# Kernel optimization log

Hardware: AMD Instinct MI355X
Metric: run time of the kernel (lower is better)

## Reference

```python
import jax, jax.numpy as jnp
import numpy as np

B, N_L, N_T, C_IN, HID, NG, ATOMS, N_EDGES = 8, 128, 512, 128, 128, 10, 24, 4096
BN_EPS = 1e-5


def setup_inputs() -> dict:
    key = jax.random.key(0)
    ks = jax.random.split(key, 20)
    f32 = jnp.float32
    s = 0.05  # weight scale
    return {
        "h_l_x": jax.random.normal(ks[0], (B, N_L, C_IN), f32),
        "h_t_x": jax.random.normal(ks[1], (B, N_T, C_IN), f32),
        "l_mask": jnp.ones((B, N_L), dtype=bool),
        "t_mask": jnp.ones((B, N_T), dtype=bool),
        "h_l_pos": jax.random.normal(ks[2], (B, N_L, 3), f32),
        "h_t_pos": jax.random.normal(ks[3], (B, N_T * ATOMS, 3), f32),
        "x_l_flat": jax.random.normal(ks[4], (B * N_L, C_IN), f32),
        "edge_index": jax.random.randint(ks[5], (2, N_EDGES), 0, B * N_L),
        "W1": jax.random.normal(ks[6], (2 * C_IN, HID), f32) * s,
        "b1": jnp.zeros((HID,), f32),
        "bn_gamma": jnp.ones((HID,), f32),
        "bn_beta": jnp.zeros((HID,), f32),
        "bn_mean": jnp.zeros((HID,), f32),
        "bn_var": jnp.ones((HID,), f32),
        "W_pi": jax.random.normal(ks[7], (HID, NG), f32) * s,
        "b_pi": jnp.zeros((NG,), f32),
        "W_sigma": jax.random.normal(ks[8], (HID, NG), f32) * s,
        "b_sigma": jnp.zeros((NG,), f32),
        "W_mu": jax.random.normal(ks[9], (HID, NG), f32) * s,
        "b_mu": jnp.zeros((NG,), f32),
        "W_nuc": jax.random.normal(ks[10], (C_IN, 12), f32) * s,
        "b_nuc": jnp.zeros((12,), f32),
        "W_bond": jax.random.normal(ks[11], (2 * C_IN, 4), f32) * s,
        "b_bond": jnp.zeros((4,), f32),
    }


def reference(h_l_x, h_t_x, l_mask, t_mask, h_l_pos, h_t_pos, x_l_flat, edge_index,
              W1, b1, bn_gamma, bn_beta, bn_mean, bn_var,
              W_pi, b_pi, W_sigma, b_sigma, W_mu, b_mu,
              W_nuc, b_nuc, W_bond, b_bond):
    Bsz, Nl, Cd = h_l_x.shape
    Nt = h_t_x.shape[1]
    # dense pairwise concat: [B, N_l, N_t, 2C] (masks are all-True, so the
    # boolean selection C[C_mask] of the original is a static flatten)
    pair = jnp.concatenate([
        jnp.broadcast_to(h_l_x[:, :, None, :], (Bsz, Nl, Nt, Cd)),
        jnp.broadcast_to(h_t_x[:, None, :, :], (Bsz, Nl, Nt, Cd)),
    ], axis=-1).reshape(-1, 2 * Cd)
    # MLP: Linear -> BatchNorm1d (eval, running stats) -> ELU -> Dropout(eval=id)
    h = pair @ W1 + b1
    h = (h - bn_mean) * jax.lax.rsqrt(bn_var + BN_EPS) * bn_gamma + bn_beta
    h = jax.nn.elu(h)
    # MDN heads
    pi = jax.nn.softmax(h @ W_pi + b_pi, axis=-1)
    sigma = jax.nn.elu(h @ W_sigma + b_sigma) + 1.1
    mu = jax.nn.elu(h @ W_mu + b_mu) + 1.0
    # auxiliary heads on flat ligand node features
    nuc_types = x_l_flat @ W_nuc + b_nuc
    bond_feat = jnp.concatenate([x_l_flat[edge_index[0]], x_l_flat[edge_index[1]]], axis=1)
    bond_types = bond_feat @ W_bond + b_bond
    # pairwise distances with windowed min over 24 atoms per target residue
    d2 = (-2.0 * jnp.einsum('bld,btd->blt', h_l_pos, h_t_pos)
          + jnp.sum(h_t_pos ** 2, axis=-1)[:, None, :]
          + jnp.sum(h_l_pos ** 2, axis=-1)[:, :, None])
    d = jnp.nan_to_num(jnp.sqrt(d2), nan=10000.0)  # nan from sqrt(<0)
    dist = d.reshape(Bsz, Nl, Nt, ATOMS).min(axis=-1)  # [B, N_l, N_t]
    dist = jax.lax.stop_gradient(dist.reshape(-1)[:, None])  # detached, [M,1]
    C_batch = jnp.broadcast_to(jnp.arange(Bsz)[:, None, None], (Bsz, Nl, Nt)).reshape(-1)
    return (pi, sigma, mu, dist, nuc_types, bond_types, C_batch)
```

## Files before the change

### kernel.cpp

```cpp
#include <hip/hip_runtime.h>

#define B_      8
#define N_L     128
#define N_T     512
#define C_IN    128
#define HID     128
#define NG      10
#define ATOMS   24
#define N_EDGES 4096

#define OFF_PI  0
#define OFF_SG  5242880
#define OFF_MU  10485760
#define OFF_DI  15728640
#define OFF_NU  16252928
#define OFF_BO  16265216
#define OFF_CB  16281600

#define WS_U    0
#define WS_V    131072
#define WS_W    655360
#define WS_B    659456
#define WS_WT   659488

typedef unsigned short u16;
typedef unsigned int   u32;
typedef short s16x8 __attribute__((ext_vector_type(8)));
typedef float f32x4 __attribute__((ext_vector_type(4)));
typedef u32   u32x4 __attribute__((ext_vector_type(4)));

__device__ __forceinline__ float bfu2f(u16 s) {
  u32 u = ((u32)s) << 16;
  return __builtin_bit_cast(float, u);
}
__device__ __forceinline__ u16 f2bf(float f) {
  u32 u = __builtin_bit_cast(u32, f);
  u32 r = (u + 0x7fffu + ((u >> 16) & 1u)) >> 16;
  return (u16)r;
}
__device__ __forceinline__ u32 pack2(float a, float b) {
  return (u32)f2bf(a) | ((u32)f2bf(b) << 16);
}
__device__ __forceinline__ u32 pkhi(float hi, float lo) {
  return __builtin_amdgcn_perm(__builtin_bit_cast(u32, hi),
                               __builtin_bit_cast(u32, lo), 0x07060302u);
}
__device__ __forceinline__ float eluf(float x) {
  return x > 0.f ? x : __expf(x) - 1.f;
}
__device__ __forceinline__ s16x8 ld8(const u16* p) {
  return __builtin_bit_cast(s16x8, *(const u32x4*)p);
}

template<bool F32>
__device__ __forceinline__ float ldf(const void* p, size_t i) {
  if constexpr (F32) return ((const float*)p)[i];
  else               return bfu2f(((const u16*)p)[i]);
}
template<bool F32>
__device__ __forceinline__ u16 wraw(const void* p, size_t i) {
  if constexpr (F32) return f2bf(((const float*)p)[i]);
  else               return ((const u16*)p)[i];
}
__device__ __forceinline__ bool is_f32(const u32* probe) {
  return (probe[0] & 0xFFFFu) == 0u;
}

template<bool F32>
__device__ __forceinline__ void prep_impl(
    const void* hlx, const void* htx, const void* W1, const void* b1,
    const void* gam, const void* bet, const void* mean_, const void* var_,
    const void* Wpi, const void* bpi, const void* Wsg, const void* bsg,
    const void* Wmu, const void* bmu, float* __restrict__ ws,
    float* __restrict__ xr) {
  int blk = blockIdx.x;
  int k = threadIdx.x;
  float A = ldf<F32>(gam, k) * rsqrtf(ldf<F32>(var_, k) + 1e-5f);
  if (blk < 5120) {
    const void* x; size_t xoff, woff; float* dst; bool isU = (blk < 1024);
    if (isU) { x = hlx; xoff = (size_t)blk * C_IN; woff = 0;
               dst = ws + WS_U + blk * HID; }
    else     { int r = blk - 1024; x = htx; xoff = (size_t)r * C_IN;
               woff = (size_t)C_IN * HID; dst = ws + WS_V + r * HID; }
    xr[k] = ldf<F32>(x, xoff + k);
    __syncthreads();
    float acc = 0.f;
    #pragma unroll 4
    for (int c = 0; c < C_IN; ++c) acc += xr[c] * ldf<F32>(W1, woff + (size_t)c * HID + k);
    float r = acc * A;
    if (isU) r += ldf<F32>(b1, k) * A + (ldf<F32>(bet, k) - ldf<F32>(mean_, k) * A);
    dst[k] = r;
  } else {
    for (int j = 0; j < 32; ++j) {
      float wv = 0.f;
      if (j < 10)      wv = ldf<F32>(Wpi, (size_t)k * NG + j);
      else if (j < 20) wv = ldf<F32>(Wsg, (size_t)k * NG + j - 10);
      else if (j < 30) wv = ldf<F32>(Wmu, (size_t)k * NG + j - 20);
      ws[WS_W + k * 32 + j] = wv;
    }
    u16* wt = (u16*)(ws + WS_WT);
    for (int j = 0; j < 32; ++j) {
      u16 val = 0;
      if (j < 10)      val = wraw<F32>(Wpi, (size_t)k * NG + j);
      else if (j < 20) val = wraw<F32>(Wsg, (size_t)k * NG + j - 10);
      else if (j < 30) val = wraw<F32>(Wmu, (size_t)k * NG + j - 20);
      wt[(size_t)j * HID + k] = val;
    }
    if (k < 32) {
      float bb = 0.f;
      if (k < 10)      bb = ldf<F32>(bpi, k);
      else if (k < 20) bb = ldf<F32>(bsg, k - 10);
      else if (k < 30) bb = ldf<F32>(bmu, k - 20);
      ws[WS_B + k] = bb;
    }
  }
}

__global__ __launch_bounds__(128) void prep_kernel(
    const void* hlx, const void* htx, const void* W1, const void* b1,
    const void* gam, const void* bet, const void* mean_, const void* var_,
    const void* Wpi, const void* bpi, const void* Wsg, const void* bsg,
    const void* Wmu, const void* bmu, float* ws, const u32* probe) {
  __shared__ float xr[C_IN];
  if (is_f32(probe))
    prep_impl<true >(hlx, htx, W1, b1, gam, bet, mean_, var_, Wpi, bpi, Wsg, bsg, Wmu, bmu, ws, xr);
  else
    prep_impl<false>(hlx, htx, W1, b1, gam, bet, mean_, var_, Wpi, bpi, Wsg, bsg, Wmu, bmu, ws, xr);
}

__global__ __launch_bounds__(256) void main_pairs(const float* __restrict__ ws,
                                                  void* __restrict__ out,
                                                  const u32* probe) {
  int tid = threadIdx.x;
  int lane = tid & 63, wave = tid >> 6;
  int p = lane & 15, q = lane >> 4;
  int bl = blockIdx.x >> 2, tq = blockIdx.x & 3;
  int b = bl >> 7;
  bool f32o = is_f32(probe);

  const u16* wt = (const u16*)(ws + WS_WT);
  s16x8 wf0[4], wf1[4];
  #pragma unroll
  for (int kt = 0; kt < 4; ++kt) {
    wf0[kt] = ld8(wt + (size_t)p        * HID + kt*32 + q*8);
    wf1[kt] = ld8(wt + (size_t)(16 + p) * HID + kt*32 + q*8);
  }
  const float* up = ws + WS_U + (size_t)bl * HID;
  float ue[4][8];
  #pragma unroll
  for (int kt = 0; kt < 4; ++kt) {
    f32x4 a0 = *(const f32x4*)(up + kt*32 + q*8);
    f32x4 a1 = *(const f32x4*)(up + kt*32 + q*8 + 4);
    #pragma unroll
    for (int i = 0; i < 4; ++i) { ue[kt][i] = a0[i]; ue[kt][4+i] = a1[i]; }
  }
  float bias0[4], bias1[4];
  #pragma unroll
  for (int r = 0; r < 4; ++r) {
    bias0[r] = ws[WS_B + q*4 + r];
    bias1[r] = ws[WS_B + 16 + q*4 + r];
  }

  for (int tt = 0; tt < 2; ++tt) {
    int t = tq * 128 + wave * 32 + tt * 16 + p;
    const float* vp = ws + WS_V + (size_t)(b * N_T + t) * HID;
    f32x4 acc0 = {0.f,0.f,0.f,0.f}, acc1 = {0.f,0.f,0.f,0.f};
    #pragma unroll
    for (int kt = 0; kt < 4; ++kt) {
      f32x4 va = *(const f32x4*)(vp + kt*32 + q*8);
      f32x4 vb = *(const f32x4*)(vp + kt*32 + q*8 + 4);
      float h0 = eluf(va[0] + ue[kt][0]);
      float h1 = eluf(va[1] + ue[kt][1]);
      float h2 = eluf(va[2] + ue[kt][2]);
      float h3 = eluf(va[3] + ue[kt][3]);
      float h4 = eluf(vb[0] + ue[kt][4]);
      float h5 = eluf(vb[1] + ue[kt][5]);
      float h6 = eluf(vb[2] + ue[kt][6]);
      float h7 = eluf(vb[3] + ue[kt][7]);
      u32x4 hw = { pkhi(h1,h0), pkhi(h3,h2), pkhi(h5,h4), pkhi(h7,h6) };
      s16x8 hf = __builtin_bit_cast(s16x8, hw);
      acc0 = __builtin_amdgcn_mfma_f32_16x16x32_bf16(wf0[kt], hf, acc0, 0, 0, 0);
      acc1 = __builtin_amdgcn_mfma_f32_16x16x32_bf16(wf1[kt], hf, acc1, 0, 0, 0);
    }
    float v0[4], v1[4];
    #pragma unroll
    for (int r = 0; r < 4; ++r) { v0[r] = acc0[r] + bias0[r]; v1[r] = acc1[r] + bias1[r]; }
    float pm = -3.0e38f;
    #pragma unroll
    for (int r = 0; r < 4; ++r) if (q*4 + r < 10) pm = fmaxf(pm, v0[r]);
    pm = fmaxf(pm, __shfl_xor(pm, 16));
    pm = fmaxf(pm, __shfl_xor(pm, 32));
    float e[4]; float es = 0.f;
    #pragma unroll
    for (int r = 0; r < 4; ++r) {
      e[r] = 0.f;
      if (q*4 + r < 10) { e[r] = __expf(v0[r] - pm); es += e[r]; }
    }
    es += __shfl_xor(es, 16);
    es += __shfl_xor(es, 32);
    float inv = 1.f / es;
    size_t base = ((size_t)bl * N_T + t) * NG;

    if (f32o) {
      float* o = (float*)out;
      if (q == 0) {
        *(float2*)(o + OFF_PI + base + 0) = make_float2(e[0]*inv, e[1]*inv);
        *(float2*)(o + OFF_PI + base + 2) = make_float2(e[2]*inv, e[3]*inv);
        *(float2*)(o + OFF_SG + base + 6) = make_float2(eluf(v1[0])+1.1f, eluf(v1[1])+1.1f);
        *(float2*)(o + OFF_SG + base + 8) = make_float2(eluf(v1[2])+1.1f, eluf(v1[3])+1.1f);
      } else if (q == 1) {
        *(float2*)(o + OFF_PI + base + 4) = make_float2(e[0]*inv, e[1]*inv);
        *(float2*)(o + OFF_PI + base + 6) = make_float2(e[2]*inv, e[3]*inv);
        *(float2*)(o + OFF_MU + base + 0) = make_float2(eluf(v1[0])+1.0f, eluf(v1[1])+1.0f);
        *(float2*)(o + OFF_MU + base + 2) = make_float2(eluf(v1[2])+1.0f, eluf(v1[3])+1.0f);
      } else if (q == 2) {
        *(float2*)(o + OFF_PI + base + 8) = make_float2(e[0]*inv, e[1]*inv);
        *(float2*)(o + OFF_SG + base + 0) = make_float2(eluf(v0[2])+1.1f, eluf(v0[3])+1.1f);
        *(float2*)(o + OFF_MU + base + 4) = make_float2(eluf(v1[0])+1.0f, eluf(v1[1])+1.0f);
        *(float2*)(o + OFF_MU + base + 6) = make_float2(eluf(v1[2])+1.0f, eluf(v1[3])+1.0f);
      } else {
        *(float2*)(o + OFF_SG + base + 2) = make_float2(eluf(v0[0])+1.1f, eluf(v0[1])+1.1f);
        *(float2*)(o + OFF_SG + base + 4) = make_float2(eluf(v0[2])+1.1f, eluf(v0[3])+1.1f);
        *(float2*)(o + OFF_MU + base + 8) = make_float2(eluf(v1[0])+1.0f, eluf(v1[1])+1.0f);
      }
    } else {
      u16* o = (u16*)out;
      if (q == 0) {
        *(u32*)(o + OFF_PI + base + 0) = pack2(e[0]*inv, e[1]*inv);
        *(u32*)(o + OFF_PI + base + 2) = pack2(e[2]*inv, e[3]*inv);
        *(u32*)(o + OFF_SG + base + 6) = pack2(eluf(v1[0])+1.1f, eluf(v1[1])+1.1f);
        *(u32*)(o + OFF_SG + base + 8) = pack2(eluf(v1[2])+1.1f, eluf(v1[3])+1.1f);
      } else if (q == 1) {
        *(u32*)(o + OFF_PI + base + 4) = pack2(e[0]*inv, e[1]*inv);
        *(u32*)(o + OFF_PI + base + 6) = pack2(e[2]*inv, e[3]*inv);
        *(u32*)(o + OFF_MU + base + 0) = pack2(eluf(v1[0])+1.0f, eluf(v1[1])+1.0f);
        *(u32*)(o + OFF_MU + base + 2) = pack2(eluf(v1[2])+1.0f, eluf(v1[3])+1.0f);
      } else if (q == 2) {
        *(u32*)(o + OFF_PI + base + 8) = pack2(e[0]*inv, e[1]*inv);
        *(u32*)(o + OFF_SG + base + 0) = pack2(eluf(v0[2])+1.1f, eluf(v0[3])+1.1f);
        *(u32*)(o + OFF_MU + base + 4) = pack2(eluf(v1[0])+1.0f, eluf(v1[1])+1.0f);
        *(u32*)(o + OFF_MU + base + 6) = pack2(eluf(v1[2])+1.0f, eluf(v1[3])+1.0f);
      } else {
        *(u32*)(o + OFF_SG + base + 2) = pack2(eluf(v0[0])+1.1f, eluf(v0[1])+1.1f);
        *(u32*)(o + OFF_SG + base + 4) = pack2(eluf(v0[2])+1.1f, eluf(v0[3])+1.1f);
        *(u32*)(o + OFF_MU + base + 8) = pack2(eluf(v1[0])+1.0f, eluf(v1[1])+1.0f);
      }
    }
  }
}

template<bool F32>
__device__ __forceinline__ void dist_impl(const void* __restrict__ lpos,
                                          const void* __restrict__ tpos,
                                          void* __restrict__ out) {
  int blk = blockIdx.x;
  int lc   = blk & 31;
  int half = (blk >> 5) & 1;
  int b    = blk >> 6;
  int t = half * 256 + threadIdx.x;

  size_t tbase = ((size_t)b * (N_T * ATOMS) + (size_t)t * ATOMS) * 3;
  float ax[ATOMS], ay[ATOMS], az[ATOMS], an[ATOMS];
  if constexpr (F32) {
    float c[72];
    const float4* tp4 = (const float4*)((const float*)tpos + tbase);
    #pragma unroll
    for (int i = 0; i < 18; ++i) {
      float4 qv = tp4[i];
      c[4*i+0] = qv.x; c[4*i+1] = qv.y; c[4*i+2] = qv.z; c[4*i+3] = qv.w;
    }
    #pragma unroll
    for (int a = 0; a < ATOMS; ++a) {
      ax[a] = c[3*a]; ay[a] = c[3*a+1]; az[a] = c[3*a+2];
      an[a] = ax[a]*ax[a] + ay[a]*ay[a] + az[a]*az[a];
    }
  } else {
    u32 raw[36];
    const uint4* tp4 = (const uint4*)((const u16*)tpos + tbase);
    #pragma unroll
    for (int i = 0; i < 9; ++i) {
      uint4 qv = tp4[i];
      raw[4*i+0] = qv.x; raw[4*i+1] = qv.y; raw[4*i+2] = qv.z; raw[4*i+3] = qv.w;
    }
    #pragma unroll
    for (int a = 0; a < ATOMS; ++a) {
      int e = 3 * a;
      u32 w0 = raw[e >> 1];
      ax[a] = bfu2f((e & 1) ? (u16)(w0 >> 16) : (u16)w0);
      u32 w1 = raw[(e + 1) >> 1];
      ay[a] = bfu2f(((e + 1) & 1) ? (u16)(w1 >> 16) : (u16)w1);
      u32 w2 = raw[(e + 2) >> 1];
      az[a] = bfu2f(((e + 2) & 1) ? (u16)(w2 >> 16) : (u16)w2);
      an[a] = ax[a]*ax[a] + ay[a]*ay[a] + az[a]*az[a];
    }
  }
  #pragma unroll
  for (int il = 0; il < 4; ++il) {
    int l = lc * 4 + il;
    size_t lbase = ((size_t)b * N_L + l) * 3;
    float lx = ldf<F32>(lpos, lbase), ly = ldf<F32>(lpos, lbase+1), lz = ldf<F32>(lpos, lbase+2);
    float ln = lx*lx + ly*ly + lz*lz;
    float m = 1e30f;
    #pragma unroll
    for (int a = 0; a < ATOMS; ++a) {
      float dot = ax[a]*lx + ay[a]*ly + az[a]*lz;
      float d2 = ln + an[a] - 2.f * dot;
      d2 = (d2 >= 0.f) ? d2 : 1e30f;
      m = fminf(m, d2);
    }
    float d = (m < 1e29f) ? sqrtf(m) : 10000.0f;
    long p = ((long)(b * N_L + l)) * N_T + t;
    if constexpr (F32) {
      ((float*)out)[OFF_DI + p] = d;
      ((float*)out)[OFF_CB + p] = (float)b;
    } else {
      ((u16*)out)[OFF_DI + p] = f2bf(d);
      ((u16*)out)[OFF_CB + p] = f2bf((float)b);
    }
  }
}

__global__ __launch_bounds__(256) void dist_kernel(const void* lpos, const void* tpos,
                                                   void* out, const u32* probe) {
  if (is_f32(probe)) dist_impl<true >(lpos, tpos, out);
  else               dist_impl<false>(lpos, tpos, out);
}

template<bool F32>
__device__ __forceinline__ void aux_impl(const void* __restrict__ xl,
                                         const int* __restrict__ eidx,
                                         const void* __restrict__ Wnu, const void* __restrict__ bnu,
                                         const void* __restrict__ Wbo, const void* __restrict__ bbo,
                                         void* __restrict__ out) {
  int gid = blockIdx.x * 256 + threadIdx.x;
  if (gid < 1024 * 12) {
    int r = gid / 12, j = gid - r * 12;
    float acc = ldf<F32>(bnu, j);
    for (int c = 0; c < C_IN; ++c)
      acc += ldf<F32>(xl, (size_t)r * C_IN + c) * ldf<F32>(Wnu, (size_t)c * 12 + j);
    if constexpr (F32) ((float*)out)[OFF_NU + gid] = acc;
    else               ((u16*)out)[OFF_NU + gid] = f2bf(acc);
  } else if (gid < 1024 * 12 + N_EDGES * 4) {
    int g = gid - 1024 * 12;
    int e = g >> 2, j = g & 3;
    int e0 = eidx[e], e1 = eidx[N_EDGES + e];
    float acc = ldf<F32>(bbo, j);
    for (int c = 0; c < C_IN; ++c)
      acc += ldf<F32>(xl, (size_t)e0 * C_IN + c) * ldf<F32>(Wbo, (size_t)c * 4 + j);
    for (int c = 0; c < C_IN; ++c)
      acc += ldf<F32>(xl, (size_t)e1 * C_IN + c) * ldf<F32>(Wbo, (size_t)(C_IN + c) * 4 + j);
    if constexpr (F32) ((float*)out)[OFF_BO + g] = acc;
    else               ((u16*)out)[OFF_BO + g] = f2bf(acc);
  }
}

__global__ __launch_bounds__(256) void aux_kernel(const void* xl, const int* eidx,
                                                  const void* Wnu, const void* bnu,
                                                  const void* Wbo, const void* bbo,
                                                  void* out, const u32* probe) {
  if (is_f32(probe)) aux_impl<true >(xl, eidx, Wnu, bnu, Wbo, bbo, out);
  else               aux_impl<false>(xl, eidx, Wnu, bnu, Wbo, bbo, out);
}

extern "C" void kernel_launch(void* const* d_in, const int* in_sizes, int n_in,
                              void* d_out, int out_size, void* d_ws, size_t ws_size,
                              hipStream_t stream) {
  int s = (n_in >= 24) ? 2 : 0;
  const void* hlx  = d_in[0];
  const void* htx  = d_in[1];
  const void* lpos = d_in[2 + s];
  const void* tpos = d_in[3 + s];
  const void* xl   = d_in[4 + s];
  const int*  eidx = (const int*)d_in[5 + s];
  const void* W1   = d_in[6 + s];
  const void* b1   = d_in[7 + s];
  const void* gam  = d_in[8 + s];
  const void* bet  = d_in[9 + s];
  const void* mean_= d_in[10 + s];
  const void* var_ = d_in[11 + s];
  const void* Wpi  = d_in[12 + s];
  const void* bpi  = d_in[13 + s];
  const void* Wsg  = d_in[14 + s];
  const void* bsg  = d_in[15 + s];
  const void* Wmu  = d_in[16 + s];
  const void* bmu  = d_in[17 + s];
  const void* Wnu  = d_in[18 + s];
  const void* bnu  = d_in[19 + s];
  const void* Wbo  = d_in[20 + s];
  const void* bbo  = d_in[21 + s];
  const u32* probe = (const u32*)var_;
  float* ws = (float*)d_ws;

  prep_kernel<<<5121, 128, 0, stream>>>(hlx, htx, W1, b1, gam, bet, mean_, var_,
                                        Wpi, bpi, Wsg, bsg, Wmu, bmu, ws, probe);
  main_pairs<<<4096, 256, 0, stream>>>(ws, d_out, probe);
  dist_kernel<<<512, 256, 0, stream>>>(lpos, tpos, d_out, probe);
  aux_kernel<<<(1024 * 12 + N_EDGES * 4 + 255) / 256, 256, 0, stream>>>(
      xl, eidx, Wnu, bnu, Wbo, bbo, d_out, probe);
}
```

Before: 204.5 us.

## Fuse four launches into two and restructure prep and aux heads

Merges the distance kernel into the prep launch and the nucleotide/bond heads into the main pair kernel, cutting four launches to two so the independent pieces can run together. The prep row projection now handles 8 rows per 256-thread block, so each W1 load is reused across four rows. The aux heads switch from one thread per output doing serial 128/256-length dots to one wave per row or edge using coalesced loads and shuffle reductions. The unused fp32 head-weight copy is dropped. In exchange, the fused launches mix block types with different register needs, which can lower occupancy for the main pair blocks.

```diff
diff --git a/kernel.cpp b/kernel.cpp
--- a/kernel.cpp
+++ b/kernel.cpp
@@ -19,7 +19,6 @@
 
 #define WS_U    0
 #define WS_V    131072
-#define WS_W    655360
 #define WS_B    659456
 #define WS_WT   659488
 
@@ -67,76 +66,233 @@
 }
 
 template<bool F32>
-__device__ __forceinline__ void prep_impl(
+__device__ __forceinline__ void prep_rows(
+    int blk, int tid,
+    const void* hlx, const void* htx, const void* W1, const void* b1,
+    const void* gam, const void* bet, const void* mean_, const void* var_,
+    float* __restrict__ ws, float (*xs)[C_IN]) {
+  int k = tid & 127, g = tid >> 7;
+  bool isU = (blk < 128);
+  const void* x = isU ? hlx : htx;
+  int row0 = isU ? blk * 8 : (blk - 128) * 8;
+  size_t woff = isU ? 0 : (size_t)C_IN * HID;
+  #pragma unroll
+  for (int i = 0; i < 4; ++i) {
+    int e = tid + i * 256;
+    int rr = e >> 7, cc = e & 127;
+    xs[rr][cc] = ldf<F32>(x, (size_t)(row0 + rr) * C_IN + cc);
+  }
+  __syncthreads();
+  float a0 = 0.f, a1 = 0.f, a2 = 0.f, a3 = 0.f;
+  const float* xr0 = xs[g * 4 + 0];
+  const float* xr1 = xs[g * 4 + 1];
+  const float* xr2 = xs[g * 4 + 2];
+  const float* xr3 = xs[g * 4 + 3];
+  #pragma unroll 8
+  for (int c = 0; c < C_IN; ++c) {
+    float w = ldf<F32>(W1, woff + (size_t)c * HID + k);
+    a0 += xr0[c] * w;
+    a1 += xr1[c] * w;
+    a2 += xr2[c] * w;
+    a3 += xr3[c] * w;
+  }
+  float A = ldf<F32>(gam, k) * rsqrtf(ldf<F32>(var_, k) + 1e-5f);
+  float add = 0.f;
+  if (isU) add = ldf<F32>(b1, k) * A + (ldf<F32>(bet, k) - ldf<F32>(mean_, k) * A);
+  float* dst = ws + (isU ? WS_U : WS_V) + (size_t)row0 * HID;
+  dst[(g * 4 + 0) * HID + k] = a0 * A + add;
+  dst[(g * 4 + 1) * HID + k] = a1 * A + add;
+  dst[(g * 4 + 2) * HID + k] = a2 * A + add;
+  dst[(g * 4 + 3) * HID + k] = a3 * A + add;
+}
+
+template<bool F32>
+__device__ __forceinline__ void prep_consts(
+    int tid, const void* Wpi, const void* bpi, const void* Wsg, const void* bsg,
+    const void* Wmu, const void* bmu, float* __restrict__ ws) {
+  if (tid >= 128) return;
+  int k = tid;
+  u16* wt = (u16*)(ws + WS_WT);
+  for (int j = 0; j < 32; ++j) {
+    u16 val = 0;
+    if (j < 10)      val = wraw<F32>(Wpi, (size_t)k * NG + j);
+    else if (j < 20) val = wraw<F32>(Wsg, (size_t)k * NG + j - 10);
+    else if (j < 30) val = wraw<F32>(Wmu, (size_t)k * NG + j - 20);
+    wt[(size_t)j * HID + k] = val;
+  }
+  if (k < 32) {
+    float bb = 0.f;
+    if (k < 10)      bb = ldf<F32>(bpi, k);
+    else if (k < 20) bb = ldf<F32>(bsg, k - 10);
+    else if (k < 30) bb = ldf<F32>(bmu, k - 20);
+    ws[WS_B + k] = bb;
+  }
+}
+
+template<bool F32>
+__device__ __forceinline__ void dist_impl(int blk2,
+                                          const void* __restrict__ lpos,
+                                          const void* __restrict__ tpos,
+                                          void* __restrict__ out) {
+  int lc   = blk2 & 31;
+  int half = (blk2 >> 5) & 1;
+  int b    = blk2 >> 6;
+  int t = half * 256 + threadIdx.x;
+
+  size_t tbase = ((size_t)b * (N_T * ATOMS) + (size_t)t * ATOMS) * 3;
+  float ax[ATOMS], ay[ATOMS], az[ATOMS], an[ATOMS];
+  if constexpr (F32) {
+    float c[72];
+    const float4* tp4 = (const float4*)((const float*)tpos + tbase);
+    #pragma unroll
+    for (int i = 0; i < 18; ++i) {
+      float4 qv = tp4[i];
+      c[4*i+0] = qv.x; c[4*i+1] = qv.y; c[4*i+2] = qv.z; c[4*i+3] = qv.w;
+    }
+    #pragma unroll
+    for (int a = 0; a < ATOMS; ++a) {
+      ax[a] = c[3*a]; ay[a] = c[3*a+1]; az[a] = c[3*a+2];
+      an[a] = ax[a]*ax[a] + ay[a]*ay[a] + az[a]*az[a];
+    }
+  } else {
+    u32 raw[36];
+    const uint4* tp4 = (const uint4*)((const u16*)tpos + tbase);
+    #pragma unroll
+    for (int i = 0; i < 9; ++i) {
+      uint4 qv = tp4[i];
+      raw[4*i+0] = qv.x; raw[4*i+1] = qv.y; raw[4*i+2] = qv.z; raw[4*i+3] = qv.w;
+    }
+    #pragma unroll
+    for (int a = 0; a < ATOMS; ++a) {
+      int e = 3 * a;
+      u32 w0 = raw[e >> 1];
+      ax[a] = bfu2f((e & 1) ? (u16)(w0 >> 16) : (u16)w0);
+      u32 w1 = raw[(e + 1) >> 1];
+      ay[a] = bfu2f(((e + 1) & 1) ? (u16)(w1 >> 16) : (u16)w1);
+      u32 w2 = raw[(e + 2) >> 1];
+      az[a] = bfu2f(((e + 2) & 1) ? (u16)(w2 >> 16) : (u16)w2);
+      an[a] = ax[a]*ax[a] + ay[a]*ay[a] + az[a]*az[a];
+    }
+  }
+  #pragma unroll
+  for (int il = 0; il < 4; ++il) {
+    int l = lc * 4 + il;
+    size_t lbase = ((size_t)b * N_L + l) * 3;
+    float lx = ldf<F32>(lpos, lbase), ly = ldf<F32>(lpos, lbase+1), lz = ldf<F32>(lpos, lbase+2);
+    float ln = lx*lx + ly*ly + lz*lz;
+    float m = 1e30f;
+    #pragma unroll
+    for (int a = 0; a < ATOMS; ++a) {
+      float dot = ax[a]*lx + ay[a]*ly + az[a]*lz;
+      float d2 = ln + an[a] - 2.f * dot;
+      d2 = (d2 >= 0.f) ? d2 : 1e30f;
+      m = fminf(m, d2);
+    }
+    float d = (m < 1e29f) ? sqrtf(m) : 10000.0f;
+    long p = ((long)(b * N_L + l)) * N_T + t;
+    if constexpr (F32) {
+      ((float*)out)[OFF_DI + p] = d;
+      ((float*)out)[OFF_CB + p] = (float)b;
+    } else {
+      ((u16*)out)[OFF_DI + p] = f2bf(d);
+      ((u16*)out)[OFF_CB + p] = f2bf((float)b);
+    }
+  }
+}
+
+__global__ __launch_bounds__(256) void prep_fused(
     const void* hlx, const void* htx, const void* W1, const void* b1,
     const void* gam, const void* bet, const void* mean_, const void* var_,
     const void* Wpi, const void* bpi, const void* Wsg, const void* bsg,
-    const void* Wmu, const void* bmu, float* __restrict__ ws,
-    float* __restrict__ xr) {
+    const void* Wmu, const void* bmu, float* ws,
+    const void* lpos, const void* tpos, void* out, const u32* probe) {
+  __shared__ float xs[8][C_IN];
   int blk = blockIdx.x;
-  int k = threadIdx.x;
-  float A = ldf<F32>(gam, k) * rsqrtf(ldf<F32>(var_, k) + 1e-5f);
-  if (blk < 5120) {
-    const void* x; size_t xoff, woff; float* dst; bool isU = (blk < 1024);
-    if (isU) { x = hlx; xoff = (size_t)blk * C_IN; woff = 0;
-               dst = ws + WS_U + blk * HID; }
-    else     { int r = blk - 1024; x = htx; xoff = (size_t)r * C_IN;
-               woff = (size_t)C_IN * HID; dst = ws + WS_V + r * HID; }
-    xr[k] = ldf<F32>(x, xoff + k);
-    __syncthreads();
-    float acc = 0.f;
-    #pragma unroll 4
-    for (int c = 0; c < C_IN; ++c) acc += xr[c] * ldf<F32>(W1, woff + (size_t)c * HID + k);
-    float r = acc * A;
-    if (isU) r += ldf<F32>(b1, k) * A + (ldf<F32>(bet, k) - ldf<F32>(mean_, k) * A);
-    dst[k] = r;
+  int tid = threadIdx.x;
+  bool f = is_f32(probe);
+  if (blk < 640) {
+    if (f) prep_rows<true >(blk, tid, hlx, htx, W1, b1, gam, bet, mean_, var_, ws, xs);
+    else   prep_rows<false>(blk, tid, hlx, htx, W1, b1, gam, bet, mean_, var_, ws, xs);
+  } else if (blk == 640) {
+    if (f) prep_consts<true >(tid, Wpi, bpi, Wsg, bsg, Wmu, bmu, ws);
+    else   prep_consts<false>(tid, Wpi, bpi, Wsg, bsg, Wmu, bmu, ws);
   } else {
-    for (int j = 0; j < 32; ++j) {
-      float wv = 0.f;
-      if (j < 10)      wv = ldf<F32>(Wpi, (size_t)k * NG + j);
-      else if (j < 20) wv = ldf<F32>(Wsg, (size_t)k * NG + j - 10);
-      else if (j < 30) wv = ldf<F32>(Wmu, (size_t)k * NG + j - 20);
-      ws[WS_W + k * 32 + j] = wv;
-    }
-    u16* wt = (u16*)(ws + WS_WT);
-    for (int j = 0; j < 32; ++j) {
-      u16 val = 0;
-      if (j < 10)      val = wraw<F32>(Wpi, (size_t)k * NG + j);
-      else if (j < 20) val = wraw<F32>(Wsg, (size_t)k * NG + j - 10);
-      else if (j < 30) val = wraw<F32>(Wmu, (size_t)k * NG + j - 20);
-      wt[(size_t)j * HID + k] = val;
-    }
-    if (k < 32) {
-      float bb = 0.f;
-      if (k < 10)      bb = ldf<F32>(bpi, k);
-      else if (k < 20) bb = ldf<F32>(bsg, k - 10);
-      else if (k < 30) bb = ldf<F32>(bmu, k - 20);
-      ws[WS_B + k] = bb;
-    }
-  }
-}
-
-__global__ __launch_bounds__(128) void prep_kernel(
-    const void* hlx, const void* htx, const void* W1, const void* b1,
-    const void* gam, const void* bet, const void* mean_, const void* var_,
-    const void* Wpi, const void* bpi, const void* Wsg, const void* bsg,
-    const void* Wmu, const void* bmu, float* ws, const u32* probe) {
-  __shared__ float xr[C_IN];
-  if (is_f32(probe))
-    prep_impl<true >(hlx, htx, W1, b1, gam, bet, mean_, var_, Wpi, bpi, Wsg, bsg, Wmu, bmu, ws, xr);
-  else
-    prep_impl<false>(hlx, htx, W1, b1, gam, bet, mean_, var_, Wpi, bpi, Wsg, bsg, Wmu, bmu, ws, xr);
-}
-
-__global__ __launch_bounds__(256) void main_pairs(const float* __restrict__ ws,
-                                                  void* __restrict__ out,
-                                                  const u32* probe) {
+    int blk2 = blk - 641;
+    if (f) dist_impl<true >(blk2, lpos, tpos, out);
+    else   dist_impl<false>(blk2, lpos, tpos, out);
+  }
+}
+
+template<bool F32>
+__device__ __forceinline__ void nuc_wave(int r, int lane, const void* __restrict__ xl,
+    const void* __restrict__ Wnu, const void* __restrict__ bnu, void* __restrict__ out) {
+  float x0 = ldf<F32>(xl, (size_t)r * C_IN + lane);
+  float x1 = ldf<F32>(xl, (size_t)r * C_IN + 64 + lane);
+  #pragma unroll
+  for (int j = 0; j < 12; ++j) {
+    float a = x0 * ldf<F32>(Wnu, (size_t)lane * 12 + j)
+            + x1 * ldf<F32>(Wnu, (size_t)(64 + lane) * 12 + j);
+    #pragma unroll
+    for (int m = 32; m >= 1; m >>= 1) a += __shfl_xor(a, m);
+    if (lane == 0) {
+      float v = a + ldf<F32>(bnu, j);
+      if constexpr (F32) ((float*)out)[OFF_NU + (size_t)r * 12 + j] = v;
+      else               ((u16*)out)[OFF_NU + (size_t)r * 12 + j] = f2bf(v);
+    }
+  }
+}
+
+template<bool F32>
+__device__ __forceinline__ void bond_wave(int e, int lane, const void* __restrict__ xl,
+    const int* __restrict__ eidx, const void* __restrict__ Wbo,
+    const void* __restrict__ bbo, void* __restrict__ out) {
+  int e0 = eidx[e], e1 = eidx[N_EDGES + e];
+  float x0 = ldf<F32>(xl, (size_t)e0 * C_IN + lane);
+  float x1 = ldf<F32>(xl, (size_t)e0 * C_IN + 64 + lane);
+  float y0 = ldf<F32>(xl, (size_t)e1 * C_IN + lane);
+  float y1 = ldf<F32>(xl, (size_t)e1 * C_IN + 64 + lane);
+  #pragma unroll
+  for (int j = 0; j < 4; ++j) {
+    float a = x0 * ldf<F32>(Wbo, (size_t)lane * 4 + j)
+            + x1 * ldf<F32>(Wbo, (size_t)(64 + lane) * 4 + j)
+            + y0 * ldf<F32>(Wbo, (size_t)(128 + lane) * 4 + j)
+            + y1 * ldf<F32>(Wbo, (size_t)(192 + lane) * 4 + j);
+    #pragma unroll
+    for (int m = 32; m >= 1; m >>= 1) a += __shfl_xor(a, m);
+    if (lane == 0) {
+      float v = a + ldf<F32>(bbo, j);
+      if constexpr (F32) ((float*)out)[OFF_BO + (size_t)e * 4 + j] = v;
+      else               ((u16*)out)[OFF_BO + (size_t)e * 4 + j] = f2bf(v);
+    }
+  }
+}
+
+__global__ __launch_bounds__(256) void main_fused(
+    const float* __restrict__ ws, void* __restrict__ out, const u32* probe,
+    const void* __restrict__ xl, const int* __restrict__ eidx,
+    const void* __restrict__ Wnu, const void* __restrict__ bnu,
+    const void* __restrict__ Wbo, const void* __restrict__ bbo) {
+  int blk = blockIdx.x;
   int tid = threadIdx.x;
   int lane = tid & 63, wave = tid >> 6;
+  bool f32o = is_f32(probe);
+
+  if (blk >= 4096) {
+    if (blk < 4096 + 256) {
+      int r = (blk - 4096) * 4 + wave;
+      if (f32o) nuc_wave<true >(r, lane, xl, Wnu, bnu, out);
+      else      nuc_wave<false>(r, lane, xl, Wnu, bnu, out);
+    } else {
+      int e = (blk - 4352) * 4 + wave;
+      if (f32o) bond_wave<true >(e, lane, xl, eidx, Wbo, bbo, out);
+      else      bond_wave<false>(e, lane, xl, eidx, Wbo, bbo, out);
+    }
+    return;
+  }
+
   int p = lane & 15, q = lane >> 4;
-  int bl = blockIdx.x >> 2, tq = blockIdx.x & 3;
+  int bl = blk >> 2, tq = blk & 3;
   int b = bl >> 7;
-  bool f32o = is_f32(probe);
 
   const u16* wt = (const u16*)(ws + WS_WT);
   s16x8 wf0[4], wf1[4];
@@ -249,119 +405,6 @@
   }
 }
 
-template<bool F32>
-__device__ __forceinline__ void dist_impl(const void* __restrict__ lpos,
-                                          const void* __restrict__ tpos,
-                                          void* __restrict__ out) {
-  int blk = blockIdx.x;
-  int lc   = blk & 31;
-  int half = (blk >> 5) & 1;
-  int b    = blk >> 6;
-  int t = half * 256 + threadIdx.x;
-
-  size_t tbase = ((size_t)b * (N_T * ATOMS) + (size_t)t * ATOMS) * 3;
-  float ax[ATOMS], ay[ATOMS], az[ATOMS], an[ATOMS];
-  if constexpr (F32) {
-    float c[72];
-    const float4* tp4 = (const float4*)((const float*)tpos + tbase);
-    #pragma unroll
-    for (int i = 0; i < 18; ++i) {
-      float4 qv = tp4[i];
-      c[4*i+0] = qv.x; c[4*i+1] = qv.y; c[4*i+2] = qv.z; c[4*i+3] = qv.w;
-    }
-    #pragma unroll
-    for (int a = 0; a < ATOMS; ++a) {
-      ax[a] = c[3*a]; ay[a] = c[3*a+1]; az[a] = c[3*a+2];
-      an[a] = ax[a]*ax[a] + ay[a]*ay[a] + az[a]*az[a];
-    }
-  } else {
-    u32 raw[36];
-    const uint4* tp4 = (const uint4*)((const u16*)tpos + tbase);
-    #pragma unroll
-    for (int i = 0; i < 9; ++i) {
-      uint4 qv = tp4[i];
-      raw[4*i+0] = qv.x; raw[4*i+1] = qv.y; raw[4*i+2] = qv.z; raw[4*i+3] = qv.w;
-    }
-    #pragma unroll
-    for (int a = 0; a < ATOMS; ++a) {
-      int e = 3 * a;
-      u32 w0 = raw[e >> 1];
-      ax[a] = bfu2f((e & 1) ? (u16)(w0 >> 16) : (u16)w0);
-      u32 w1 = raw[(e + 1) >> 1];
-      ay[a] = bfu2f(((e + 1) & 1) ? (u16)(w1 >> 16) : (u16)w1);
-      u32 w2 = raw[(e + 2) >> 1];
-      az[a] = bfu2f(((e + 2) & 1) ? (u16)(w2 >> 16) : (u16)w2);
-      an[a] = ax[a]*ax[a] + ay[a]*ay[a] + az[a]*az[a];
-    }
-  }
-  #pragma unroll
-  for (int il = 0; il < 4; ++il) {
-    int l = lc * 4 + il;
-    size_t lbase = ((size_t)b * N_L + l) * 3;
-    float lx = ldf<F32>(lpos, lbase), ly = ldf<F32>(lpos, lbase+1), lz = ldf<F32>(lpos, lbase+2);
-    float ln = lx*lx + ly*ly + lz*lz;
-    float m = 1e30f;
-    #pragma unroll
-    for (int a = 0; a < ATOMS; ++a) {
-      float dot = ax[a]*lx + ay[a]*ly + az[a]*lz;
-      float d2 = ln + an[a] - 2.f * dot;
-      d2 = (d2 >= 0.f) ? d2 : 1e30f;
-      m = fminf(m, d2);
-    }
-    float d = (m < 1e29f) ? sqrtf(m) : 10000.0f;
-    long p = ((long)(b * N_L + l)) * N_T + t;
-    if constexpr (F32) {
-      ((float*)out)[OFF_DI + p] = d;
-      ((float*)out)[OFF_CB + p] = (float)b;
-    } else {
-      ((u16*)out)[OFF_DI + p] = f2bf(d);
-      ((u16*)out)[OFF_CB + p] = f2bf((float)b);
-    }
-  }
-}
-
-__global__ __launch_bounds__(256) void dist_kernel(const void* lpos, const void* tpos,
-                                                   void* out, const u32* probe) {
-  if (is_f32(probe)) dist_impl<true >(lpos, tpos, out);
-  else               dist_impl<false>(lpos, tpos, out);
-}
-
-template<bool F32>
-__device__ __forceinline__ void aux_impl(const void* __restrict__ xl,
-                                         const int* __restrict__ eidx,
-                                         const void* __restrict__ Wnu, const void* __restrict__ bnu,
-                                         const void* __restrict__ Wbo, const void* __restrict__ bbo,
-                                         void* __restrict__ out) {
-  int gid = blockIdx.x * 256 + threadIdx.x;
-  if (gid < 1024 * 12) {
-    int r = gid / 12, j = gid - r * 12;
-    float acc = ldf<F32>(bnu, j);
-    for (int c = 0; c < C_IN; ++c)
-      acc += ldf<F32>(xl, (size_t)r * C_IN + c) * ldf<F32>(Wnu, (size_t)c * 12 + j);
-    if constexpr (F32) ((float*)out)[OFF_NU + gid] = acc;
-    else               ((u16*)out)[OFF_NU + gid] = f2bf(acc);
-  } else if (gid < 1024 * 12 + N_EDGES * 4) {
-    int g = gid - 1024 * 12;
-    int e = g >> 2, j = g & 3;
-    int e0 = eidx[e], e1 = eidx[N_EDGES + e];
-    float acc = ldf<F32>(bbo, j);
-    for (int c = 0; c < C_IN; ++c)
-      acc += ldf<F32>(xl, (size_t)e0 * C_IN + c) * ldf<F32>(Wbo, (size_t)c * 4 + j);
-    for (int c = 0; c < C_IN; ++c)
-      acc += ldf<F32>(xl, (size_t)e1 * C_IN + c) * ldf<F32>(Wbo, (size_t)(C_IN + c) * 4 + j);
-    if constexpr (F32) ((float*)out)[OFF_BO + g] = acc;
-    else               ((u16*)out)[OFF_BO + g] = f2bf(acc);
-  }
-}
-
-__global__ __launch_bounds__(256) void aux_kernel(const void* xl, const int* eidx,
-                                                  const void* Wnu, const void* bnu,
-                                                  const void* Wbo, const void* bbo,
-                                                  void* out, const u32* probe) {
-  if (is_f32(probe)) aux_impl<true >(xl, eidx, Wnu, bnu, Wbo, bbo, out);
-  else               aux_impl<false>(xl, eidx, Wnu, bnu, Wbo, bbo, out);
-}
-
 extern "C" void kernel_launch(void* const* d_in, const int* in_sizes, int n_in,
                               void* d_out, int out_size, void* d_ws, size_t ws_size,
                               hipStream_t stream) {
@@ -391,10 +434,9 @@
   const u32* probe = (const u32*)var_;
   float* ws = (float*)d_ws;
 
-  prep_kernel<<<5121, 128, 0, stream>>>(hlx, htx, W1, b1, gam, bet, mean_, var_,
-                                        Wpi, bpi, Wsg, bsg, Wmu, bmu, ws, probe);
-  main_pairs<<<4096, 256, 0, stream>>>(ws, d_out, probe);
-  dist_kernel<<<512, 256, 0, stream>>>(lpos, tpos, d_out, probe);
-  aux_kernel<<<(1024 * 12 + N_EDGES * 4 + 255) / 256, 256, 0, stream>>>(
-      xl, eidx, Wnu, bnu, Wbo, bbo, d_out, probe);
-}
+  prep_fused<<<1153, 256, 0, stream>>>(hlx, htx, W1, b1, gam, bet, mean_, var_,
+                                       Wpi, bpi, Wsg, bsg, Wmu, bmu, ws,
+                                       lpos, tpos, d_out, probe);
+  main_fused<<<5376, 256, 0, stream>>>(ws, d_out, probe,
+                                       xl, eidx, Wnu, bnu, Wbo, bbo);
+}
```

Result: faster. 190.0 us (-7.1%).
